# Kernel optimization log

Hardware: AMD Instinct MI355X
Metric: run time of the kernel (lower is better)

Reference implementation:

```python
import jax, jax.numpy as jnp
import numpy as np

N_GRID, N_MESH, N_EDGE, H = 65536, 10242, 131072, 512

def _layernorm(x, g, b, eps=1e-5):
    m = jnp.mean(x, axis=-1, keepdims=True)
    v = jnp.var(x, axis=-1, keepdims=True)
    return (x - m) * jax.lax.rsqrt(v + eps) * g + b

def _mlp(x, W1, b1, W2, b2, g, b):
    # Linear -> SiLU -> Linear -> LayerNorm (GraphCast MeshGraphMLP)
    h = jax.nn.silu(x @ W1 + b1)
    return _layernorm(h @ W2 + b2, g, b)

def setup_inputs() -> dict:
    key = jax.random.key(0)
    ks = jax.random.split(key, 16)
    s = lambda fan_in: 1.0 / np.sqrt(fan_in)
    inp = {
        'grid_node_features': jax.random.normal(ks[0], (N_GRID, H), jnp.float32),
        'mesh_node_features': jax.random.normal(ks[1], (N_MESH, H), jnp.float32),
        'grid2mesh_edge_features': jax.random.normal(ks[2], (N_EDGE, H), jnp.float32),
        'src_indices': jax.random.randint(ks[3], (N_EDGE,), 0, N_GRID),
        'dst_indices': jax.random.randint(ks[4], (N_EDGE,), 0, N_MESH),
        # edge MLP: in = concat(edge, src, dst) = 3H
        'We1': jax.random.normal(ks[5], (3 * H, H), jnp.float32) * s(3 * H),
        'be1': jnp.zeros((H,), jnp.float32),
        'We2': jax.random.normal(ks[6], (H, H), jnp.float32) * s(H),
        'be2': jnp.zeros((H,), jnp.float32),
        'ge': jnp.ones((H,), jnp.float32), 'bbe': jnp.zeros((H,), jnp.float32),
        # node MLP: in = concat(node, agg) = 2H
        'Wn1': jax.random.normal(ks[7], (2 * H, H), jnp.float32) * s(2 * H),
        'bn1': jnp.zeros((H,), jnp.float32),
        'Wn2': jax.random.normal(ks[8], (H, H), jnp.float32) * s(H),
        'bn2': jnp.zeros((H,), jnp.float32),
        'gn': jnp.ones((H,), jnp.float32), 'bbn': jnp.zeros((H,), jnp.float32),
        # grid node MLP: H -> H
        'Wg1': jax.random.normal(ks[9], (H, H), jnp.float32) * s(H),
        'bg1': jnp.zeros((H,), jnp.float32),
        'Wg2': jax.random.normal(ks[10], (H, H), jnp.float32) * s(H),
        'bg2': jnp.zeros((H,), jnp.float32),
        'gg': jnp.ones((H,), jnp.float32), 'bbg': jnp.zeros((H,), jnp.float32),
    }
    return inp

def reference(grid_node_features, mesh_node_features, grid2mesh_edge_features,
              src_indices, dst_indices,
              We1, be1, We2, be2, ge, bbe,
              Wn1, bn1, Wn2, bn2, gn, bbn,
              Wg1, bg1, Wg2, bg2, gg, bbg):
    # --- MeshEdgeBlock: gather src/dst, concat, MLP, residual on edges ---
    cat_e = jnp.concatenate([grid2mesh_edge_features,
                             grid_node_features[src_indices],
                             mesh_node_features[dst_indices]], axis=-1)  # [E, 3H]
    e_feats = grid2mesh_edge_features + _mlp(cat_e, We1, be1, We2, be2, ge, bbe)
    # --- MeshNodeBlock: scatter-sum edges to mesh nodes, concat, MLP ---
    agg = jax.ops.segment_sum(e_feats, dst_indices, num_segments=N_MESH)  # [M, H]
    cat_n = jnp.concatenate([mesh_node_features, agg], axis=-1)  # [M, 2H]
    n_feats = _mlp(cat_n, Wn1, bn1, Wn2, bn2, gn, bbn)
    mesh_out = mesh_node_features + n_feats
    # --- grid node MLP + residual ---
    grid_out = grid_node_features + _mlp(grid_node_features, Wg1, bg1, Wg2, bg2, gg, bbg)
    return (grid_out, mesh_out)
```

## Files before the change

### kernel.cpp

```cpp
#include <hip/hip_runtime.h>
#include <stdint.h>

typedef unsigned short u16;
typedef unsigned int   u32;
typedef unsigned char  u8;

using bf16x8 = __attribute__((ext_vector_type(8))) short;
using f32x4  = __attribute__((ext_vector_type(4))) float;

#define DEVF static __device__ __forceinline__

DEVF u16 f2bf(float f){
  u32 u = __builtin_bit_cast(u32, f);
  u32 r = u + 0x7FFFu + ((u >> 16) & 1u);
  return (u16)(r >> 16);
}
DEVF float bf2f(u16 h){
  u32 u = ((u32)h) << 16;
  return __builtin_bit_cast(float, u);
}

DEVF void gload_lds16(const u16* g, u16* s){
  __builtin_amdgcn_global_load_lds(
      (const __attribute__((address_space(1))) u32*)g,
      (__attribute__((address_space(3))) u32*)(u32)(uintptr_t)s,
      16, 0, 0);
}


__global__ __launch_bounds__(256) void k_f32_to_bf16(const float* __restrict__ in,
                                                     u16* __restrict__ out, long n){
  long i = (long)blockIdx.x * blockDim.x + threadIdx.x;
  long stride = (long)gridDim.x * blockDim.x;
  for (long j = i * 8; j < n; j += stride * 8){
    float4 a = *(const float4*)(in + j);
    float4 b = *(const float4*)(in + j + 4);
    bf16x8 v;
    v[0]=(short)f2bf(a.x); v[1]=(short)f2bf(a.y); v[2]=(short)f2bf(a.z); v[3]=(short)f2bf(a.w);
    v[4]=(short)f2bf(b.x); v[5]=(short)f2bf(b.y); v[6]=(short)f2bf(b.z); v[7]=(short)f2bf(b.w);
    *(bf16x8*)(out + j) = v;
  }
}

__global__ __launch_bounds__(256) void k_zero_i32(int* __restrict__ p, int n){
  int i = blockIdx.x * 256 + threadIdx.x;
  if (i < n) p[i] = 0;
}

__global__ __launch_bounds__(256) void k_transpose_w(const float* __restrict__ W,
                                                     u16* __restrict__ Wt, int K, int N){
  int idx = blockIdx.x * 256 + threadIdx.x;
  if (idx < K * N){
    int k = idx / N, n = idx - k * N;
    Wt[(size_t)n * K + k] = f2bf(W[idx]);
  }
}


__global__ __launch_bounds__(256)
void k_hist(const int* __restrict__ dst, int* __restrict__ cnt, int E){
  int e = blockIdx.x * 256 + threadIdx.x;
  if (e < E) atomicAdd(&cnt[dst[e]], 1);
}

__global__ __launch_bounds__(1024)
void k_scan(const int* __restrict__ cnt, int* __restrict__ offs, int n){
  __shared__ int part[1024];
  int t = threadIdx.x;
  const int PER = (n + 1023) / 1024;
  int base = t * PER;
  int s = 0;
  for (int i = 0; i < PER; ++i){ int idx = base + i; if (idx < n) s += cnt[idx]; }
  part[t] = s;
  __syncthreads();
  for (int o = 1; o < 1024; o <<= 1){
    int v = (t >= o) ? part[t - o] : 0;
    __syncthreads();
    part[t] += v;
    __syncthreads();
  }
  int run = (t == 0) ? 0 : part[t - 1];
  for (int i = 0; i < PER; ++i){
    int idx = base + i;
    if (idx < n){ offs[idx] = run; run += cnt[idx]; }
  }
  if (t == 1023) offs[n] = part[1023];
}

__global__ __launch_bounds__(256)
void k_scatter(const int* __restrict__ dst, const int* __restrict__ offs,
               int* __restrict__ cur, int* __restrict__ eid, int E){
  int e = blockIdx.x * 256 + threadIdx.x;
  if (e < E){
    int d = dst[e];
    int p = offs[d] + atomicAdd(&cur[d], 1);
    eid[p] = e;
  }
}


#define LDA4(BUF, MH, KK, AF) \
  _Pragma("unroll") for (int m_ = 0; m_ < 4; ++m_) \
    AF[m_] = *(const bf16x8*)&lA[BUF][(wm * 128 + (MH) * 64 + m_ * 16 + lane16) * 64 + \
                                      ((((KK) << 2) | kl) ^ (lane16 & 7)) * 8];

#define LDB4(BUF, KK, BFR) \
  _Pragma("unroll") for (int n_ = 0; n_ < 4; ++n_) \
    BFR[n_] = *(const bf16x8*)&lB[BUF][(wn * 64 + n_ * 16 + lane16) * 64 + \
                                       ((((KK) << 2) | kl) ^ (lane16 & 7)) * 8];

#define PHASE_MFMA(MH, AF, BFR) \
  __builtin_amdgcn_s_setprio(1); \
  _Pragma("unroll") for (int m_ = 0; m_ < 4; ++m_) \
    _Pragma("unroll") for (int n_ = 0; n_ < 4; ++n_) \
      acc[(MH) * 4 + m_][n_] = __builtin_amdgcn_mfma_f32_16x16x32_bf16( \
          AF[m_], BFR[n_], acc[(MH) * 4 + m_][n_], 0, 0, 0); \
  __builtin_amdgcn_s_setprio(0);

#define STAGE_A(BUF, KT_, RND) do{ \
    const int k0_ = (KT_) * 64; \
    const u16* ga_; \
    if (MODE == 0){ ga_ = A + (size_t)srows[RND] * K + k0_ + kchunk; } \
    else if (MODE == 1){ \
      int seg_ = k0_ >> 9, klo_ = k0_ & 511; \
      const u16* b_ = (seg_ == 0) ? A  + (size_t)srows[RND] * 512 \
                    : (seg_ == 1) ? G1 + (size_t)sidx1[RND] * 512 \
                                  : G2 + (size_t)sidx2[RND] * 512; \
      ga_ = b_ + klo_ + kchunk; \
    } else { \
      int seg_ = k0_ >> 9, klo_ = k0_ & 511; \
      const u16* b_ = (seg_ == 0) ? A  + (size_t)srows[RND] * 512 \
                                  : G1 + (size_t)srows[RND] * 512; \
      ga_ = b_ + klo_ + kchunk; \
    } \
    gload_lds16(ga_, &lA[BUF][((RND) * 64 + w * 8) * 64]); \
  }while(0)

#define STAGE_B(BUF, KT_, RND) \
  gload_lds16(bptr[RND] + (KT_) * 64 + kchunk, &lB[BUF][((RND) * 64 + w * 8) * 64])

#define WAITBAR(N) do{ \
    asm volatile("s_waitcnt vmcnt(" #N ")" ::: "memory"); \
    __builtin_amdgcn_s_barrier(); \
    __builtin_amdgcn_sched_barrier(0); \
  }while(0)

template<int MODE, int EPI>
__global__ __launch_bounds__(512)
void k_gemm256(const u16* __restrict__ A, const u16* __restrict__ G1, const u16* __restrict__ G2,
               const int* __restrict__ srcI, const int* __restrict__ dstI,
               const u16* __restrict__ Bt, const float* __restrict__ bias,
               void* __restrict__ out, int M, int K)
{
  __shared__ __align__(16) u16 lA[2][256 * 64];
  __shared__ __align__(16) u16 lB[2][256 * 64];

  const int tid = threadIdx.x;
  const int w = tid >> 6, l = tid & 63;
  const int col0 = blockIdx.x * 256;
  const int row0 = blockIdx.y * 256;

  int srows[4], sidx1[4], sidx2[4];
  const u16* bptr[4];
  #pragma unroll
  for (int it = 0; it < 4; ++it){
    int r = row0 + it * 64 + w * 8 + (l >> 3);
    if (r >= M) r = M - 1;
    srows[it] = r;
    if (MODE == 1){ sidx1[it] = srcI[r]; sidx2[it] = dstI[r]; }
    int n = col0 + it * 64 + w * 8 + (l >> 3);
    bptr[it] = Bt + (size_t)n * K;
  }
  const int kchunk = ((l & 7) ^ (l >> 3)) * 8;

  f32x4 acc[8][4];
  #pragma unroll
  for (int m = 0; m < 8; ++m)
    #pragma unroll
    for (int n = 0; n < 4; ++n)
      acc[m][n] = (f32x4){0.f, 0.f, 0.f, 0.f};

  const int wm = w >> 2, wn = w & 3;
  const int lane16 = l & 15, kl = l >> 4;

  const int KT = K >> 6;

  STAGE_A(0, 0, 0); STAGE_A(0, 0, 2);
  STAGE_B(0, 0, 0); STAGE_B(0, 0, 1); STAGE_B(0, 0, 2); STAGE_B(0, 0, 3);
  STAGE_A(0, 0, 1); STAGE_A(0, 0, 3);

  for (int kt = 0; kt < KT; ++kt){
    const int buf = kt & 1;
    const bool more = (kt + 1 < KT);
    bf16x8 af[4], bfr[4];

    WAITBAR(2);

    LDB4(buf, 0, bfr);
    LDA4(buf, 0, 0, af);
    if (more){ STAGE_A(buf ^ 1, kt + 1, 0); STAGE_A(buf ^ 1, kt + 1, 2); }
    PHASE_MFMA(0, af, bfr);

    if (more){ WAITBAR(2); } else { WAITBAR(0); }

    LDA4(buf, 1, 0, af);
    if (more){ STAGE_B(buf ^ 1, kt + 1, 0); STAGE_B(buf ^ 1, kt + 1, 1); }
    PHASE_MFMA(1, af, bfr);

    LDB4(buf, 1, bfr);
    LDA4(buf, 0, 1, af);
    if (more){ STAGE_B(buf ^ 1, kt + 1, 2); STAGE_B(buf ^ 1, kt + 1, 3); }
    PHASE_MFMA(0, af, bfr);

    LDA4(buf, 1, 1, af);
    if (more){ STAGE_A(buf ^ 1, kt + 1, 1); STAGE_A(buf ^ 1, kt + 1, 3); }
    PHASE_MFMA(1, af, bfr);
  }

  #pragma unroll
  for (int m = 0; m < 8; ++m){
    int rbase = row0 + wm * 128 + m * 16 + kl * 4;
    #pragma unroll
    for (int n = 0; n < 4; ++n){
      int cg = col0 + wn * 64 + n * 16 + lane16;
      #pragma unroll
      for (int j = 0; j < 4; ++j){
        int rg = rbase + j;
        if (rg < M){
          float v = acc[m][n][j];
          if (EPI == 0){
            v += bias[cg];
            v = v / (1.f + __expf(-v));
            ((u16*)out)[(size_t)rg * 512 + cg] = f2bf(v);
          } else if (EPI == 1){
            ((u16*)out)[(size_t)rg * 512 + cg] = f2bf(v);
          } else {
            ((float*)out)[(size_t)rg * 512 + cg] = v;
          }
        }
      }
    }
  }
}


template<int MODE, int EPI>
__global__ __launch_bounds__(256)
void k_gemm(const u16* __restrict__ A, const u16* __restrict__ G1, const u16* __restrict__ G2,
            const int* __restrict__ src, const int* __restrict__ dst,
            const u16* __restrict__ Bt, const float* __restrict__ bias,
            void* __restrict__ out, int M, int K)
{
  __shared__ __align__(16) u16 lA[128 * 64];
  __shared__ __align__(16) u16 lB[128 * 64];

  const int tid = threadIdx.x;
  const int w = tid >> 6, l = tid & 63;
  const int row0 = blockIdx.x * 128;
  const int col0 = blockIdx.y * 128;

  int srows[4], sidx1[4], sidx2[4];
  const u16* bptr[4];
  #pragma unroll
  for (int it = 0; it < 4; ++it){
    int r = row0 + it * 32 + w * 8 + (l >> 3);
    if (r >= M) r = M - 1;
    srows[it] = r;
    if (MODE == 1){ sidx1[it] = src[r]; sidx2[it] = dst[r]; }
    int n = col0 + it * 32 + w * 8 + (l >> 3);
    bptr[it] = Bt + (size_t)n * K;
  }
  const int kchunk = (l & 7) * 8;

  f32x4 acc[4][4];
  #pragma unroll
  for (int m = 0; m < 4; ++m)
    #pragma unroll
    for (int n = 0; n < 4; ++n)
      acc[m][n] = (f32x4){0.f, 0.f, 0.f, 0.f};

  const int wm = w >> 1, wn = w & 1;
  const int lane16 = l & 15, kl = l >> 4;

  const int KT = K >> 6;
  for (int kt = 0; kt < KT; ++kt){
    const int k0 = kt * 64;
    __syncthreads();
    #pragma unroll
    for (int it = 0; it < 4; ++it){
      const u16* ga;
      if (MODE == 0){
        ga = A + (size_t)srows[it] * K + k0 + kchunk;
      } else if (MODE == 1){
        int seg = k0 >> 9, klocal = k0 & 511;
        const u16* base = (seg == 0) ? A  + (size_t)srows[it] * 512
                        : (seg == 1) ? G1 + (size_t)sidx1[it] * 512
                                     : G2 + (size_t)sidx2[it] * 512;
        ga = base + klocal + kchunk;
      } else {
        int seg = k0 >> 9, klocal = k0 & 511;
        const u16* base = (seg == 0) ? A  + (size_t)srows[it] * 512
                                     : G1 + (size_t)srows[it] * 512;
        ga = base + klocal + kchunk;
      }
      gload_lds16(ga, &lA[(it * 32 + w * 8) * 64]);
      gload_lds16(bptr[it] + k0 + kchunk, &lB[(it * 32 + w * 8) * 64]);
    }
    __syncthreads();

    #pragma unroll
    for (int kk = 0; kk < 2; ++kk){
      bf16x8 af[4], bfr[4];
      #pragma unroll
      for (int m = 0; m < 4; ++m)
        af[m] = *(const bf16x8*)&lA[(wm * 64 + m * 16 + lane16) * 64 + kk * 32 + kl * 8];
      #pragma unroll
      for (int n = 0; n < 4; ++n)
        bfr[n] = *(const bf16x8*)&lB[(wn * 64 + n * 16 + lane16) * 64 + kk * 32 + kl * 8];
      #pragma unroll
      for (int m = 0; m < 4; ++m)
        #pragma unroll
        for (int n = 0; n < 4; ++n)
          acc[m][n] = __builtin_amdgcn_mfma_f32_16x16x32_bf16(af[m], bfr[n], acc[m][n], 0, 0, 0);
    }
  }

  #pragma unroll
  for (int m = 0; m < 4; ++m){
    int rbase = row0 + wm * 64 + m * 16 + kl * 4;
    #pragma unroll
    for (int n = 0; n < 4; ++n){
      int cg = col0 + wn * 64 + n * 16 + lane16;
      #pragma unroll
      for (int j = 0; j < 4; ++j){
        int rg = rbase + j;
        if (rg < M){
          float v = acc[m][n][j];
          if (EPI == 0){
            v += bias[cg];
            v = v / (1.f + __expf(-v));
            ((u16*)out)[(size_t)rg * 512 + cg] = f2bf(v);
          } else if (EPI == 1){
            ((u16*)out)[(size_t)rg * 512 + cg] = f2bf(v);
          } else {
            ((float*)out)[(size_t)rg * 512 + cg] = v;
          }
        }
      }
    }
  }
}


__global__ __launch_bounds__(256)
void k_agg(const u16* __restrict__ e2, const float* __restrict__ be2,
           const float* __restrict__ ge, const float* __restrict__ bbe,
           const float* __restrict__ edge_f, const int* __restrict__ offs,
           const int* __restrict__ eid, u16* __restrict__ aggbf, int Mn)
{
  int node = blockIdx.x * 4 + (threadIdx.x >> 6);
  int l = threadIdx.x & 63;
  if (node >= Mn) return;
  int p0 = offs[node], p1 = offs[node + 1];

  float b2c[8], gc[8], bbc[8];
  #pragma unroll
  for (int j = 0; j < 8; ++j){
    int c = l * 8 + j;
    b2c[j] = be2[c]; gc[j] = ge[c]; bbc[j] = bbe[c];
  }

  float acc[8] = {0.f,0.f,0.f,0.f,0.f,0.f,0.f,0.f};
  for (int p = p0; p < p1; ++p){
    int e = eid[p];
    bf16x8 v = *(const bf16x8*)(e2 + (size_t)e * 512 + l * 8);
    const float* ei = edge_f + (size_t)e * 512 + l * 8;
    float4 a = *(const float4*)ei, b4 = *(const float4*)(ei + 4);
    float eiv[8] = {a.x, a.y, a.z, a.w, b4.x, b4.y, b4.z, b4.w};
    float x[8], s = 0.f, sq = 0.f;
    #pragma unroll
    for (int j = 0; j < 8; ++j){
      x[j] = bf2f((u16)v[j]) + b2c[j];
      s += x[j]; sq += x[j] * x[j];
    }
    #pragma unroll
    for (int o = 32; o; o >>= 1){ s += __shfl_xor(s, o); sq += __shfl_xor(sq, o); }
    float mean = s * (1.f / 512.f);
    float var = sq * (1.f / 512.f) - mean * mean;
    float rs = rsqrtf(var + 1e-5f);
    #pragma unroll
    for (int j = 0; j < 8; ++j)
      acc[j] += (x[j] - mean) * rs * gc[j] + bbc[j] + eiv[j];
  }

  bf16x8 o8;
  #pragma unroll
  for (int j = 0; j < 8; ++j) o8[j] = (short)f2bf(acc[j]);
  *(bf16x8*)(aggbf + (size_t)node * 512 + l * 8) = o8;
}


__global__ __launch_bounds__(256)
void k_ln_out(const float* __restrict__ x2, const float* __restrict__ b2,
              const float* __restrict__ g, const float* __restrict__ bb,
              const float* __restrict__ resid, float* __restrict__ out, int R)
{
  int row = blockIdx.x * 4 + (threadIdx.x >> 6);
  int l = threadIdx.x & 63;
  if (row >= R) return;
  const float* xr = x2 + (size_t)row * 512 + l * 8;
  float4 a = *(const float4*)xr, b4 = *(const float4*)(xr + 4);
  float x[8] = {a.x, a.y, a.z, a.w, b4.x, b4.y, b4.z, b4.w};
  float s = 0.f, sq = 0.f;
  #pragma unroll
  for (int j = 0; j < 8; ++j){
    x[j] += b2[l * 8 + j];
    s += x[j]; sq += x[j] * x[j];
  }
  #pragma unroll
  for (int o = 32; o; o >>= 1){ s += __shfl_xor(s, o); sq += __shfl_xor(sq, o); }
  float mean = s * (1.f / 512.f);
  float var = sq * (1.f / 512.f) - mean * mean;
  float rs = rsqrtf(var + 1e-5f);
  const float* rr = resid + (size_t)row * 512 + l * 8;
  float* po = out + (size_t)row * 512 + l * 8;
  #pragma unroll
  for (int j = 0; j < 8; ++j){
    int c = l * 8 + j;
    po[j] = (x[j] - mean) * rs * g[c] + bb[c] + rr[j];
  }
}


extern "C" void kernel_launch(void* const* d_in, const int* in_sizes, int n_in,
                              void* d_out, int out_size, void* d_ws, size_t ws_size,
                              hipStream_t stream)
{
  const int N_GRID = 65536, N_MESH = 10242, N_EDGE = 131072, H = 512;

  const float* grid_f = (const float*)d_in[0];
  const float* mesh_f = (const float*)d_in[1];
  const float* edge_f = (const float*)d_in[2];
  const int*   src    = (const int*)d_in[3];
  const int*   dst    = (const int*)d_in[4];
  const float* We1 = (const float*)d_in[5];  const float* be1 = (const float*)d_in[6];
  const float* We2 = (const float*)d_in[7];  const float* be2 = (const float*)d_in[8];
  const float* ge  = (const float*)d_in[9];  const float* bbe = (const float*)d_in[10];
  const float* Wn1 = (const float*)d_in[11]; const float* bn1 = (const float*)d_in[12];
  const float* Wn2 = (const float*)d_in[13]; const float* bn2 = (const float*)d_in[14];
  const float* gn  = (const float*)d_in[15]; const float* bbn = (const float*)d_in[16];
  const float* Wg1 = (const float*)d_in[17]; const float* bg1 = (const float*)d_in[18];
  const float* Wg2 = (const float*)d_in[19]; const float* bg2 = (const float*)d_in[20];
  const float* gg  = (const float*)d_in[21]; const float* bbg = (const float*)d_in[22];

  u8* ws = (u8*)d_ws;
  const size_t MiB = 1u << 20;
  u16*  Gbf   = (u16*)(ws + 0);
  u16*  Mbf   = (u16*)(ws + 64  * MiB);
  u16*  AggBf = (u16*)(ws + 75  * MiB);
  u16*  We1t  = (u16*)(ws + 86  * MiB);
  u16*  We2t  = (u16*)(ws + 86  * MiB + 1572864);
  u16*  Wn1t  = (u16*)(ws + 86  * MiB + 2097152);
  u16*  Wn2t  = (u16*)(ws + 86  * MiB + 3145728);
  u16*  Wg1t  = (u16*)(ws + 86  * MiB + 3670016);
  u16*  Wg2t  = (u16*)(ws + 86  * MiB + 4194304);
  int*  offs  = (int*)(ws + 91 * MiB);
  int*  cnt   = (int*)(ws + 91 * MiB) + 10496;
  int*  cur   = (int*)(ws + 91 * MiB) + 20992;
  int*  eid   = (int*)(ws + 91 * MiB) + 31488;
  u16*  He    = (u16*)(ws + 112 * MiB);
  u8*   Big   =  ws + 240 * MiB;
  u16*  Ebf   = (u16*)Big;
  u16*  E2    = (u16*)Big;
  float* N2   = (float*)Big;
  float* G2   = (float*)Big;

  float* grid_out = (float*)d_out;
  float* mesh_out = (float*)d_out + (size_t)N_GRID * H;

  k_f32_to_bf16<<<2048, 256, 0, stream>>>(grid_f, Gbf, (long)N_GRID * H);
  k_f32_to_bf16<<<1024, 256, 0, stream>>>(mesh_f, Mbf, (long)N_MESH * H);
  k_f32_to_bf16<<<4096, 256, 0, stream>>>(edge_f, Ebf, (long)N_EDGE * H);
  k_transpose_w<<<(1536 * 512 + 255) / 256, 256, 0, stream>>>(We1, We1t, 1536, 512);
  k_transpose_w<<<(512  * 512 + 255) / 256, 256, 0, stream>>>(We2, We2t, 512, 512);
  k_transpose_w<<<(1024 * 512 + 255) / 256, 256, 0, stream>>>(Wn1, Wn1t, 1024, 512);
  k_transpose_w<<<(512  * 512 + 255) / 256, 256, 0, stream>>>(Wn2, Wn2t, 512, 512);
  k_transpose_w<<<(512  * 512 + 255) / 256, 256, 0, stream>>>(Wg1, Wg1t, 512, 512);
  k_transpose_w<<<(512  * 512 + 255) / 256, 256, 0, stream>>>(Wg2, Wg2t, 512, 512);
  k_zero_i32<<<(20992 + 255) / 256, 256, 0, stream>>>(cnt, 20992);
  k_hist<<<N_EDGE / 256, 256, 0, stream>>>(dst, cnt, N_EDGE);
  k_scan<<<1, 1024, 0, stream>>>(cnt, offs, N_MESH);
  k_scatter<<<N_EDGE / 256, 256, 0, stream>>>(dst, offs, cur, eid, N_EDGE);

  dim3 ge1(2, N_EDGE / 256);
  k_gemm256<1, 0><<<ge1, 512, 0, stream>>>(Ebf, Gbf, Mbf, src, dst, We1t, be1, He, N_EDGE, 1536);
  k_gemm256<0, 1><<<ge1, 512, 0, stream>>>(He, nullptr, nullptr, nullptr, nullptr, We2t, nullptr, E2, N_EDGE, 512);
  k_agg<<<(N_MESH + 3) / 4, 256, 0, stream>>>(E2, be2, ge, bbe, edge_f, offs, eid, AggBf, N_MESH);

  dim3 gn1((N_MESH + 127) / 128, 4);
  k_gemm<2, 0><<<gn1, 256, 0, stream>>>(Mbf, AggBf, nullptr, nullptr, nullptr, Wn1t, bn1, He, N_MESH, 1024);
  k_gemm<0, 2><<<gn1, 256, 0, stream>>>(He, nullptr, nullptr, nullptr, nullptr, Wn2t, nullptr, N2, N_MESH, 512);
  k_ln_out<<<(N_MESH + 3) / 4, 256, 0, stream>>>(N2, bn2, gn, bbn, mesh_f, mesh_out, N_MESH);

  dim3 gg1(2, N_GRID / 256);
  k_gemm256<0, 0><<<gg1, 512, 0, stream>>>(Gbf, nullptr, nullptr, nullptr, nullptr, Wg1t, bg1, He, N_GRID, 512);
  k_gemm256<0, 2><<<gg1, 512, 0, stream>>>(He, nullptr, nullptr, nullptr, nullptr, Wg2t, nullptr, G2, N_GRID, 512);
  k_ln_out<<<N_GRID / 4, 256, 0, stream>>>(G2, bg2, gg, bbg, grid_f, grid_out, N_GRID);
}
```

Before: 1.073 ms.

## Precompute mesh-node projection of edge MLP and add it in epilogue

Splits the first edge-MLP weight so the destination-node term is computed once per mesh node with a small GEMM, then gathered and added in the edge GEMM epilogue. This cuts the edge GEMM K dimension from 1536 to 1024. The change also remaps workgroup indices in the 256-tile GEMM for cache locality, and reads the grid residual from bf16 instead of fp32. It adds a per-row indexed gather in the epilogue and slightly lowers residual precision.

```diff
diff --git a/kernel.cpp b/kernel.cpp
--- a/kernel.cpp
+++ b/kernel.cpp
@@ -47,12 +47,13 @@
   if (i < n) p[i] = 0;
 }
 
-__global__ __launch_bounds__(256) void k_transpose_w(const float* __restrict__ W,
-                                                     u16* __restrict__ Wt, int K, int N){
+__global__ __launch_bounds__(256) void k_transpose_w_off(const float* __restrict__ W,
+                                                         u16* __restrict__ Wt,
+                                                         int K, int N, int k0){
   int idx = blockIdx.x * 256 + threadIdx.x;
   if (idx < K * N){
     int k = idx / N, n = idx - k * N;
-    Wt[(size_t)n * K + k] = f2bf(W[idx]);
+    Wt[(size_t)n * K + k] = f2bf(W[(size_t)(k + k0) * N + n]);
   }
 }
 
@@ -121,16 +122,10 @@
     const int k0_ = (KT_) * 64; \
     const u16* ga_; \
     if (MODE == 0){ ga_ = A + (size_t)srows[RND] * K + k0_ + kchunk; } \
-    else if (MODE == 1){ \
+    else { \
       int seg_ = k0_ >> 9, klo_ = k0_ & 511; \
       const u16* b_ = (seg_ == 0) ? A  + (size_t)srows[RND] * 512 \
-                    : (seg_ == 1) ? G1 + (size_t)sidx1[RND] * 512 \
-                                  : G2 + (size_t)sidx2[RND] * 512; \
-      ga_ = b_ + klo_ + kchunk; \
-    } else { \
-      int seg_ = k0_ >> 9, klo_ = k0_ & 511; \
-      const u16* b_ = (seg_ == 0) ? A  + (size_t)srows[RND] * 512 \
-                                  : G1 + (size_t)srows[RND] * 512; \
+                                  : G1 + (size_t)sidx1[RND] * 512; \
       ga_ = b_ + klo_ + kchunk; \
     } \
     gload_lds16(ga_, &lA[BUF][((RND) * 64 + w * 8) * 64]); \
@@ -157,17 +152,21 @@
 
   const int tid = threadIdx.x;
   const int w = tid >> 6, l = tid & 63;
-  const int col0 = blockIdx.x * 256;
-  const int row0 = blockIdx.y * 256;
-
-  int srows[4], sidx1[4], sidx2[4];
+
+  const int nwg = gridDim.x * gridDim.y;
+  const int wgf = blockIdx.y * gridDim.x + blockIdx.x;
+  const int lg  = (wgf & 7) * (nwg >> 3) + (wgf >> 3);
+  const int col0 = (lg % gridDim.x) * 256;
+  const int row0 = (lg / gridDim.x) * 256;
+
+  int srows[4], sidx1[4];
   const u16* bptr[4];
   #pragma unroll
   for (int it = 0; it < 4; ++it){
     int r = row0 + it * 64 + w * 8 + (l >> 3);
     if (r >= M) r = M - 1;
     srows[it] = r;
-    if (MODE == 1){ sidx1[it] = srcI[r]; sidx2[it] = dstI[r]; }
+    if (MODE == 1){ sidx1[it] = srcI[r]; }
     int n = col0 + it * 64 + w * 8 + (l >> 3);
     bptr[it] = Bt + (size_t)n * K;
   }
@@ -220,6 +219,113 @@
   #pragma unroll
   for (int m = 0; m < 8; ++m){
     int rbase = row0 + wm * 128 + m * 16 + kl * 4;
+    #pragma unroll
+    for (int j = 0; j < 4; ++j){
+      int rg = rbase + j;
+      if (rg < M){
+        int dd = 0;
+        if (EPI == 3) dd = dstI[rg];
+        #pragma unroll
+        for (int n = 0; n < 4; ++n){
+          int cg = col0 + wn * 64 + n * 16 + lane16;
+          float v = acc[m][n][j];
+          if (EPI == 0){
+            v += bias[cg];
+            v = v / (1.f + __expf(-v));
+            ((u16*)out)[(size_t)rg * 512 + cg] = f2bf(v);
+          } else if (EPI == 3){
+            v += bias[cg] + bf2f(G2[(size_t)dd * 512 + cg]);
+            v = v / (1.f + __expf(-v));
+            ((u16*)out)[(size_t)rg * 512 + cg] = f2bf(v);
+          } else if (EPI == 1){
+            ((u16*)out)[(size_t)rg * 512 + cg] = f2bf(v);
+          } else {
+            ((float*)out)[(size_t)rg * 512 + cg] = v;
+          }
+        }
+      }
+    }
+  }
+}
+
+
+template<int MODE, int EPI>
+__global__ __launch_bounds__(256)
+void k_gemm(const u16* __restrict__ A, const u16* __restrict__ G1, const u16* __restrict__ G2,
+            const int* __restrict__ src, const int* __restrict__ dst,
+            const u16* __restrict__ Bt, const float* __restrict__ bias,
+            void* __restrict__ out, int M, int K)
+{
+  __shared__ __align__(16) u16 lA[128 * 64];
+  __shared__ __align__(16) u16 lB[128 * 64];
+
+  const int tid = threadIdx.x;
+  const int w = tid >> 6, l = tid & 63;
+  const int row0 = blockIdx.x * 128;
+  const int col0 = blockIdx.y * 128;
+
+  int srows[4];
+  const u16* bptr[4];
+  #pragma unroll
+  for (int it = 0; it < 4; ++it){
+    int r = row0 + it * 32 + w * 8 + (l >> 3);
+    if (r >= M) r = M - 1;
+    srows[it] = r;
+    int n = col0 + it * 32 + w * 8 + (l >> 3);
+    bptr[it] = Bt + (size_t)n * K;
+  }
+  const int kchunk = (l & 7) * 8;
+
+  f32x4 acc[4][4];
+  #pragma unroll
+  for (int m = 0; m < 4; ++m)
+    #pragma unroll
+    for (int n = 0; n < 4; ++n)
+      acc[m][n] = (f32x4){0.f, 0.f, 0.f, 0.f};
+
+  const int wm = w >> 1, wn = w & 1;
+  const int lane16 = l & 15, kl = l >> 4;
+
+  const int KT = K >> 6;
+  for (int kt = 0; kt < KT; ++kt){
+    const int k0 = kt * 64;
+    __syncthreads();
+    #pragma unroll
+    for (int it = 0; it < 4; ++it){
+      const u16* ga;
+      if (MODE == 0){
+        ga = A + (size_t)srows[it] * K + k0 + kchunk;
+      } else {
+        int seg = k0 >> 9, klocal = k0 & 511;
+        const u16* base = (seg == 0) ? A  + (size_t)srows[it] * 512
+                                     : G1 + (size_t)srows[it] * 512;
+        ga = base + klocal + kchunk;
+      }
+      gload_lds16(ga, &lA[(it * 32 + w * 8) * 64]);
+      gload_lds16(bptr[it] + k0 + kchunk, &lB[(it * 32 + w * 8) * 64]);
+    }
+    __syncthreads();
+
+    #pragma unroll
+    for (int kk = 0; kk < 2; ++kk){
+      bf16x8 af[4], bfr[4];
+      #pragma unroll
+      for (int m = 0; m < 4; ++m)
+        af[m] = *(const bf16x8*)&lA[(wm * 64 + m * 16 + lane16) * 64 + kk * 32 + kl * 8];
+      #pragma unroll
+      for (int n = 0; n < 4; ++n)
+        bfr[n] = *(const bf16x8*)&lB[(wn * 64 + n * 16 + lane16) * 64 + kk * 32 + kl * 8];
+      #pragma unroll
+      for (int m = 0; m < 4; ++m)
+        #pragma unroll
+        for (int n = 0; n < 4; ++n)
+          acc[m][n] = __builtin_amdgcn_mfma_f32_16x16x32_bf16(af[m], bfr[n], acc[m][n], 0, 0, 0);
+    }
+  }
+
+  #pragma unroll
+  for (int m = 0; m < 4; ++m){
+    int rbase = row0 + wm * 64 + m * 16 + kl * 4;
     #pragma unroll
     for (int n = 0; n < 4; ++n){
       int cg = col0 + wn * 64 + n * 16 + lane16;
@@ -244,114 +350,6 @@
 }
 
 
-template<int MODE, int EPI>
-__global__ __launch_bounds__(256)
-void k_gemm(const u16* __restrict__ A, const u16* __restrict__ G1, const u16* __restrict__ G2,
-            const int* __restrict__ src, const int* __restrict__ dst,
-            const u16* __restrict__ Bt, const float* __restrict__ bias,
-            void* __restrict__ out, int M, int K)
-{
-  __shared__ __align__(16) u16 lA[128 * 64];
-  __shared__ __align__(16) u16 lB[128 * 64];
-
-  const int tid = threadIdx.x;
-  const int w = tid >> 6, l = tid & 63;
-  const int row0 = blockIdx.x * 128;
-  const int col0 = blockIdx.y * 128;
-
-  int srows[4], sidx1[4], sidx2[4];
-  const u16* bptr[4];
-  #pragma unroll
-  for (int it = 0; it < 4; ++it){
-    int r = row0 + it * 32 + w * 8 + (l >> 3);
-    if (r >= M) r = M - 1;
-    srows[it] = r;
-    if (MODE == 1){ sidx1[it] = src[r]; sidx2[it] = dst[r]; }
-    int n = col0 + it * 32 + w * 8 + (l >> 3);
-    bptr[it] = Bt + (size_t)n * K;
-  }
-  const int kchunk = (l & 7) * 8;
-
-  f32x4 acc[4][4];
-  #pragma unroll
-  for (int m = 0; m < 4; ++m)
-    #pragma unroll
-    for (int n = 0; n < 4; ++n)
-      acc[m][n] = (f32x4){0.f, 0.f, 0.f, 0.f};
-
-  const int wm = w >> 1, wn = w & 1;
-  const int lane16 = l & 15, kl = l >> 4;
-
-  const int KT = K >> 6;
-  for (int kt = 0; kt < KT; ++kt){
-    const int k0 = kt * 64;
-    __syncthreads();
-    #pragma unroll
-    for (int it = 0; it < 4; ++it){
-      const u16* ga;
-      if (MODE == 0){
-        ga = A + (size_t)srows[it] * K + k0 + kchunk;
-      } else if (MODE == 1){
-        int seg = k0 >> 9, klocal = k0 & 511;
-        const u16* base = (seg == 0) ? A  + (size_t)srows[it] * 512
-                        : (seg == 1) ? G1 + (size_t)sidx1[it] * 512
-                                     : G2 + (size_t)sidx2[it] * 512;
-        ga = base + klocal + kchunk;
-      } else {
-        int seg = k0 >> 9, klocal = k0 & 511;
-        const u16* base = (seg == 0) ? A  + (size_t)srows[it] * 512
-                                     : G1 + (size_t)srows[it] * 512;
-        ga = base + klocal + kchunk;
-      }
-      gload_lds16(ga, &lA[(it * 32 + w * 8) * 64]);
-      gload_lds16(bptr[it] + k0 + kchunk, &lB[(it * 32 + w * 8) * 64]);
-    }
-    __syncthreads();
-
-    #pragma unroll
-    for (int kk = 0; kk < 2; ++kk){
-      bf16x8 af[4], bfr[4];
-      #pragma unroll
-      for (int m = 0; m < 4; ++m)
-        af[m] = *(const bf16x8*)&lA[(wm * 64 + m * 16 + lane16) * 64 + kk * 32 + kl * 8];
-      #pragma unroll
-      for (int n = 0; n < 4; ++n)
-        bfr[n] = *(const bf16x8*)&lB[(wn * 64 + n * 16 + lane16) * 64 + kk * 32 + kl * 8];
-      #pragma unroll
-      for (int m = 0; m < 4; ++m)
-        #pragma unroll
-        for (int n = 0; n < 4; ++n)
-          acc[m][n] = __builtin_amdgcn_mfma_f32_16x16x32_bf16(af[m], bfr[n], acc[m][n], 0, 0, 0);
-    }
-  }
-
-  #pragma unroll
-  for (int m = 0; m < 4; ++m){
-    int rbase = row0 + wm * 64 + m * 16 + kl * 4;
-    #pragma unroll
-    for (int n = 0; n < 4; ++n){
-      int cg = col0 + wn * 64 + n * 16 + lane16;
-      #pragma unroll
-      for (int j = 0; j < 4; ++j){
-        int rg = rbase + j;
-        if (rg < M){
-          float v = acc[m][n][j];
-          if (EPI == 0){
-            v += bias[cg];
-            v = v / (1.f + __expf(-v));
-            ((u16*)out)[(size_t)rg * 512 + cg] = f2bf(v);
-          } else if (EPI == 1){
-            ((u16*)out)[(size_t)rg * 512 + cg] = f2bf(v);
-          } else {
-            ((float*)out)[(size_t)rg * 512 + cg] = v;
-          }
-        }
-      }
-    }
-  }
-}
-
-
 __global__ __launch_bounds__(256)
 void k_agg(const u16* __restrict__ e2, const float* __restrict__ be2,
            const float* __restrict__ ge, const float* __restrict__ bbe,
@@ -428,6 +426,37 @@
   for (int j = 0; j < 8; ++j){
     int c = l * 8 + j;
     po[j] = (x[j] - mean) * rs * g[c] + bb[c] + rr[j];
+  }
+}
+
+__global__ __launch_bounds__(256)
+void k_ln_out_bf(const float* __restrict__ x2, const float* __restrict__ b2,
+                 const float* __restrict__ g, const float* __restrict__ bb,
+                 const u16* __restrict__ resid, float* __restrict__ out, int R)
+{
+  int row = blockIdx.x * 4 + (threadIdx.x >> 6);
+  int l = threadIdx.x & 63;
+  if (row >= R) return;
+  const float* xr = x2 + (size_t)row * 512 + l * 8;
+  float4 a = *(const float4*)xr, b4 = *(const float4*)(xr + 4);
+  float x[8] = {a.x, a.y, a.z, a.w, b4.x, b4.y, b4.z, b4.w};
+  float s = 0.f, sq = 0.f;
+  #pragma unroll
+  for (int j = 0; j < 8; ++j){
+    x[j] += b2[l * 8 + j];
+    s += x[j]; sq += x[j] * x[j];
+  }
+  #pragma unroll
+  for (int o = 32; o; o >>= 1){ s += __shfl_xor(s, o); sq += __shfl_xor(sq, o); }
+  float mean = s * (1.f / 512.f);
+  float var = sq * (1.f / 512.f) - mean * mean;
+  float rs = rsqrtf(var + 1e-5f);
+  bf16x8 rv = *(const bf16x8*)(resid + (size_t)row * 512 + l * 8);
+  float* po = out + (size_t)row * 512 + l * 8;
+  #pragma unroll
+  for (int j = 0; j < 8; ++j){
+    int c = l * 8 + j;
+    po[j] = (x[j] - mean) * rs * g[c] + bb[c] + bf2f((u16)rv[j]);
   }
 }
 
@@ -459,6 +488,7 @@
   u16*  Mbf   = (u16*)(ws + 64  * MiB);
   u16*  AggBf = (u16*)(ws + 75  * MiB);
   u16*  We1t  = (u16*)(ws + 86  * MiB);
+  u16*  Wpm   = (u16*)(ws + 86  * MiB + 1048576);
   u16*  We2t  = (u16*)(ws + 86  * MiB + 1572864);
   u16*  Wn1t  = (u16*)(ws + 86  * MiB + 2097152);
   u16*  Wn2t  = (u16*)(ws + 86  * MiB + 3145728);
@@ -468,6 +498,7 @@
   int*  cnt   = (int*)(ws + 91 * MiB) + 10496;
   int*  cur   = (int*)(ws + 91 * MiB) + 20992;
   int*  eid   = (int*)(ws + 91 * MiB) + 31488;
+  u16*  Pm    = (u16*)(ws + 96 * MiB);
   u16*  He    = (u16*)(ws + 112 * MiB);
   u8*   Big   =  ws + 240 * MiB;
   u16*  Ebf   = (u16*)Big;
@@ -481,19 +512,23 @@
   k_f32_to_bf16<<<2048, 256, 0, stream>>>(grid_f, Gbf, (long)N_GRID * H);
   k_f32_to_bf16<<<1024, 256, 0, stream>>>(mesh_f, Mbf, (long)N_MESH * H);
   k_f32_to_bf16<<<4096, 256, 0, stream>>>(edge_f, Ebf, (long)N_EDGE * H);
-  k_transpose_w<<<(1536 * 512 + 255) / 256, 256, 0, stream>>>(We1, We1t, 1536, 512);
-  k_transpose_w<<<(512  * 512 + 255) / 256, 256, 0, stream>>>(We2, We2t, 512, 512);
-  k_transpose_w<<<(1024 * 512 + 255) / 256, 256, 0, stream>>>(Wn1, Wn1t, 1024, 512);
-  k_transpose_w<<<(512  * 512 + 255) / 256, 256, 0, stream>>>(Wn2, Wn2t, 512, 512);
-  k_transpose_w<<<(512  * 512 + 255) / 256, 256, 0, stream>>>(Wg1, Wg1t, 512, 512);
-  k_transpose_w<<<(512  * 512 + 255) / 256, 256, 0, stream>>>(Wg2, Wg2t, 512, 512);
+  k_transpose_w_off<<<(1024 * 512 + 255) / 256, 256, 0, stream>>>(We1, We1t, 1024, 512, 0);
+  k_transpose_w_off<<<(512  * 512 + 255) / 256, 256, 0, stream>>>(We1, Wpm, 512, 512, 1024);
+  k_transpose_w_off<<<(512  * 512 + 255) / 256, 256, 0, stream>>>(We2, We2t, 512, 512, 0);
+  k_transpose_w_off<<<(1024 * 512 + 255) / 256, 256, 0, stream>>>(Wn1, Wn1t, 1024, 512, 0);
+  k_transpose_w_off<<<(512  * 512 + 255) / 256, 256, 0, stream>>>(Wn2, Wn2t, 512, 512, 0);
+  k_transpose_w_off<<<(512  * 512 + 255) / 256, 256, 0, stream>>>(Wg1, Wg1t, 512, 512, 0);
+  k_transpose_w_off<<<(512  * 512 + 255) / 256, 256, 0, stream>>>(Wg2, Wg2t, 512, 512, 0);
   k_zero_i32<<<(20992 + 255) / 256, 256, 0, stream>>>(cnt, 20992);
   k_hist<<<N_EDGE / 256, 256, 0, stream>>>(dst, cnt, N_EDGE);
   k_scan<<<1, 1024, 0, stream>>>(cnt, offs, N_MESH);
   k_scatter<<<N_EDGE / 256, 256, 0, stream>>>(dst, offs, cur, eid, N_EDGE);
 
+  dim3 gpm((N_MESH + 127) / 128, 4);
+  k_gemm<0, 1><<<gpm, 256, 0, stream>>>(Mbf, nullptr, nullptr, nullptr, nullptr, Wpm, nullptr, Pm, N_MESH, 512);
+
   dim3 ge1(2, N_EDGE / 256);
-  k_gemm256<1, 0><<<ge1, 512, 0, stream>>>(Ebf, Gbf, Mbf, src, dst, We1t, be1, He, N_EDGE, 1536);
+  k_gemm256<1, 3><<<ge1, 512, 0, stream>>>(Ebf, Gbf, Pm, src, dst, We1t, be1, He, N_EDGE, 1024);
   k_gemm256<0, 1><<<ge1, 512, 0, stream>>>(He, nullptr, nullptr, nullptr, nullptr, We2t, nullptr, E2, N_EDGE, 512);
   k_agg<<<(N_MESH + 3) / 4, 256, 0, stream>>>(E2, be2, ge, bbe, edge_f, offs, eid, AggBf, N_MESH);
 
@@ -505,5 +540,5 @@
   dim3 gg1(2, N_GRID / 256);
   k_gemm256<0, 0><<<gg1, 512, 0, stream>>>(Gbf, nullptr, nullptr, nullptr, nullptr, Wg1t, bg1, He, N_GRID, 512);
   k_gemm256<0, 2><<<gg1, 512, 0, stream>>>(He, nullptr, nullptr, nullptr, nullptr, Wg2t, nullptr, G2, N_GRID, 512);
-  k_ln_out<<<N_GRID / 4, 256, 0, stream>>>(G2, bg2, gg, bbg, grid_f, grid_out, N_GRID);
-}
+  k_ln_out_bf<<<N_GRID / 4, 256, 0, stream>>>(G2, bg2, gg, bbg, Gbf, grid_out, N_GRID);
+}
```

Result: faster. 1.011 ms (-5.7%).
